# Kernel tuning notes

Measured on AMD Instinct MI355X. Metric: run time of the kernel, lower is better.

Reference implementation:

```python
import jax, jax.numpy as jnp
import numpy as np

B, S, H, F, E, K = 2, 2048, 1024, 4096, 8, 2


def setup_inputs() -> dict:
    key = jax.random.key(0)
    ks = jax.random.split(key, 6)
    x = jax.random.normal(ks[0], (B, S, H), dtype=jnp.float32)
    probs = jax.random.uniform(ks[1], (K, B, S, 1), dtype=jnp.float32)
    experts = jax.random.randint(ks[2], (K, B, S, 1), 0, E, dtype=jnp.int32)
    # per-expert FFN params; 0.02 scale mimics typical transformer init
    w1 = jax.random.normal(ks[3], (E, H, F), dtype=jnp.float32) * 0.02
    b1 = jnp.zeros((E, F), dtype=jnp.float32)
    w2 = jax.random.normal(ks[4], (E, F, H), dtype=jnp.float32) * 0.02
    b2 = jnp.zeros((E, H), dtype=jnp.float32)
    return {"x": x, "probs": probs, "experts": experts,
            "w1": w1, "b1": b1, "w2": w2, "b2": b2}


def reference(x, probs, experts, w1, b1, w2, b2):
    # Dense compute-all-experts FFN: every expert processes every token.
    h = jnp.einsum('bsh,ehf->ebsf', x, w1) + b1[:, None, None, :]  # [E,B,S,F]
    h = jax.nn.gelu(h)
    y = jnp.einsum('ebsf,efh->ebsh', h, w2) + b2[:, None, None, :]  # [E,B,S,H]
    # Masked combine: sum_e sum_j probs_j * y_e * (experts_j == e)
    onehot = jax.nn.one_hot(experts[..., 0], w1.shape[0], dtype=x.dtype)  # [K,B,S,E]
    weights = jnp.einsum('kbsl,kbse->bse', probs, onehot)  # [B,S,E]
    out = jnp.einsum('bse,ebsh->bsh', weights, y)
    return out
```

## Files before the change

### kernel.cpp

```cpp
#include <hip/hip_runtime.h>
#include <stdint.h>

#define H_DIM 1024
#define F_DIM 4096
#define E_NUM 8
#define T_NUM 4096
#define NE    8192
#define BM    256
#define BN    256
#define BK    64
#define MAXT  40
#define PADM  9984
#define TBY   65536
#define LDSSZ (2*TBY)

#define G1_NWG (MAXT * (F_DIM / BN))
#define TRW2_NWG 4096
#define TRW1_NWG 4096

#define M_NT  0
#define M_PB  1
#define M_CNT 16
#define M_CUR 24
#define M_TE  32
#define M_TR  72
#define M_INTS 112

typedef float  f32x4  __attribute__((ext_vector_type(4)));
typedef short  bf16x8 __attribute__((ext_vector_type(8)));
typedef __bf16 b16v8  __attribute__((ext_vector_type(8)));
typedef unsigned short u16;
typedef u16    u16x8  __attribute__((ext_vector_type(8)));

#define BAR()   __builtin_amdgcn_s_barrier()
#define FENCE() asm volatile("" ::: "memory")
#define LGKM0() asm volatile("s_waitcnt lgkmcnt(0)" ::: "memory")

__device__ __forceinline__ float gelu_tanh(float v) {
  float u = 0.7978845608028654f * (v + 0.044715f * v * v * v);
  return v / (1.0f + __expf(-2.0f * u));
}

__device__ __forceinline__ float b2f(u16 v) {
  union { float f; unsigned u; } x; x.u = ((unsigned)v) << 16; return x.f;
}

__device__ __forceinline__ void gl16(const void* g, void* l) {
  __builtin_amdgcn_global_load_lds(
      (const __attribute__((address_space(1))) unsigned int*)g,
      (__attribute__((address_space(3))) unsigned int*)l, 16, 0, 0);
}

__device__ __forceinline__ void trans_tile(const float* __restrict__ W, u16* __restrict__ Wt,
                                           int R, int C, int e, int bx, int by,
                                           char* L, int tid) {
  int r0 = by * 64, c0 = bx * 64;
  const float* We = W + (size_t)e * R * C;
  u16* Wte = Wt + (size_t)e * R * C;
#pragma unroll
  for (int it = 0; it < 4; ++it) {
    int gi = it * 256 + tid;
    int row = gi >> 4, c4 = gi & 15;
    f32x4 v = *(const f32x4*)(We + (size_t)(r0 + row) * C + c0 + c4 * 4);
    *(f32x4*)(L + row * 256 + ((c4 ^ (row & 15)) * 16)) = v;
  }
  __syncthreads();
#pragma unroll
  for (int s = 0; s < 2; ++s) {
    int chunk = s * 256 + tid;
    int c = chunk >> 3, rb = chunk & 7;
    b16v8 o;
#pragma unroll
    for (int j = 0; j < 8; ++j) {
      int r = rb * 8 + j;
      float f = *(const float*)(L + r * 256 + (((c >> 2) ^ (r & 15)) * 16) + (c & 3) * 4);
      o[j] = (__bf16)f;
    }
    *(b16v8*)(void*)(Wte + (size_t)(c0 + c) * R + r0 + rb * 8) = o;
  }
}


__global__ void k_init(int* tok, float* wgt, int* meta) {
  int i = blockIdx.x * 256 + threadIdx.x;
  if (i < PADM) { tok[i] = 0; wgt[i] = 0.f; }
  if (i < E_NUM) { meta[M_CNT + i] = 0; meta[M_CUR + i] = 0; }
}

__global__ void k_count(const int* __restrict__ experts, int* meta) {
  int i = blockIdx.x * 256 + threadIdx.x;
  int e = experts[i];
  int lane = threadIdx.x & 63;
#pragma unroll
  for (int ee = 0; ee < E_NUM; ++ee) {
    unsigned long long bm = __ballot(e == ee);
    if (e == ee && lane == __builtin_ctzll(bm))
      atomicAdd(&meta[M_CNT + ee], __popcll(bm));
  }
}

__global__ void k_plan(int* meta) {
  if (threadIdx.x != 0 || blockIdx.x != 0) return;
  int pb = 0, idx = 0;
  for (int e = 0; e < E_NUM; ++e) {
    int c = meta[M_CNT + e];
    int nt = (c + BM - 1) / BM;
    meta[M_PB + e] = pb;
    for (int t = 0; t < nt && idx < MAXT; ++t) {
      meta[M_TE + idx] = e; meta[M_TR + idx] = pb + t * BM; ++idx;
    }
    pb += nt * BM;
  }
  meta[M_NT] = idx;
}

__global__ void k_scatter(const int* __restrict__ experts, const float* __restrict__ probs,
                          int* tok, float* wgt, int* entpos, int* meta) {
  int i = blockIdx.x * 256 + threadIdx.x;
  int e = experts[i];
  int t = i & (T_NUM - 1);
  float p = probs[i];
  int lane = threadIdx.x & 63;
#pragma unroll
  for (int ee = 0; ee < E_NUM; ++ee) {
    unsigned long long bm = __ballot(e == ee);
    if (e == ee) {
      int leader = __builtin_ctzll(bm);
      int cnt = __popcll(bm);
      int base = 0;
      if (lane == leader) base = atomicAdd(&meta[M_CUR + ee], cnt);
      base = __shfl(base, leader);
      int rank = __popcll(bm & ((1ull << lane) - 1ull));
      int pos = meta[M_PB + ee] + base + rank;
      tok[pos] = t;
      wgt[pos] = p;
      entpos[i] = pos;
    }
  }
}

__global__ __launch_bounds__(512) void k_prep(const float* __restrict__ x, u16* __restrict__ xbf,
                                              const float* __restrict__ w1, u16* __restrict__ w1t) {
  int bid = blockIdx.x;
  if (bid < TRW1_NWG) {
    alignas(16) __shared__ char L[32768];
    int ti = bid * 2 + (threadIdx.x >> 8);
    int e = ti >> 10, rem = ti & 1023;
    int bx = rem & 63, by = rem >> 6;
    trans_tile(w1, w1t, H_DIM, F_DIM, e, bx, by, L + (threadIdx.x >> 8) * 16384, threadIdx.x & 255);
    return;
  }
  int i = (bid - TRW1_NWG) * 512 + threadIdx.x;
  const f32x4* xp = (const f32x4*)x;
  f32x4 a = xp[i * 2], b = xp[i * 2 + 1];
  b16v8 o;
  o[0] = (__bf16)a[0]; o[1] = (__bf16)a[1]; o[2] = (__bf16)a[2]; o[3] = (__bf16)a[3];
  o[4] = (__bf16)b[0]; o[5] = (__bf16)b[1]; o[6] = (__bf16)b[2]; o[7] = (__bf16)b[3];
  ((b16v8*)xbf)[i] = o;
}

__global__ __launch_bounds__(256) void k_trans(const float* __restrict__ W, u16* __restrict__ Wt,
                                               int R, int C) {
  alignas(16) __shared__ char L[16384];
  trans_tile(W, Wt, R, C, blockIdx.z, blockIdx.x, blockIdx.y, L, threadIdx.x);
}


#define STG_A(kt, dbb, h)                                                     \
  { gl16(asrc[2*(h)]   + (size_t)(kt) * BK, LDS + (dbb) + (2*(h))   * 8192 + wid * 1024); \
    gl16(asrc[2*(h)+1] + (size_t)(kt) * BK, LDS + (dbb) + (2*(h)+1) * 8192 + wid * 1024); }
#define STG_B(kt, dbb, h)                                                     \
  { gl16(bsrc[2*(h)]   + (size_t)(kt) * BK, LDS + (dbb) + 32768 + (2*(h))   * 8192 + wid * 1024); \
    gl16(bsrc[2*(h)+1] + (size_t)(kt) * BK, LDS + (dbb) + 32768 + (2*(h)+1) * 8192 + wid * 1024); }

#define LD_A(dst, mi, kk)                                                     \
  { int r_ = wr * 128 + (mi) * 16 + (lane & 15);                              \
    int kb_ = (kk) * 64 + ((lane >> 4) << 4);                                 \
    dst = *(const bf16x8*)(Ab_ + r_ * 128 + (kb_ ^ ((r_ & 7) << 4))); }
#define LD_B(dst, ni, kk)                                                     \
  { int c_ = wc * 64 + (ni) * 16 + (lane & 15);                               \
    int kb_ = (kk) * 64 + ((lane >> 4) << 4);                                 \
    dst = *(const bf16x8*)(Bb_ + c_ * 128 + (kb_ ^ ((c_ & 7) << 4))); }

#define MFMA16(p)                                                             \
  __builtin_amdgcn_s_setprio(1);                                              \
  _Pragma("unroll") for (int mm = 0; mm < 2; ++mm)                            \
    _Pragma("unroll") for (int n = 0; n < 4; ++n) {                           \
      acc[2*(p)+mm][n] = __builtin_amdgcn_mfma_f32_16x16x32_bf16(af[mm][0], bfr[n][0], acc[2*(p)+mm][n], 0, 0, 0); \
      acc[2*(p)+mm][n] = __builtin_amdgcn_mfma_f32_16x16x32_bf16(af[mm][1], bfr[n][1], acc[2*(p)+mm][n], 0, 0, 0); \
    }                                                                         \
  __builtin_amdgcn_s_setprio(0);

#define GEMM_KLOOP_8P(NT)                                                     \
  STG_A(0, 0, 0); STG_A(0, 0, 1); STG_B(0, 0, 0); STG_B(0, 0, 1);             \
  STG_B(1, TBY, 0); STG_B(1, TBY, 1);                                         \
  asm volatile("s_waitcnt vmcnt(4)" ::: "memory");                            \
  BAR();                                                                      \
  { int cur = 0;                                                              \
    for (int kt = 0; kt < (NT); ++kt) {                                       \
      const int db = cur * TBY, dn = (cur ^ 1) * TBY;                         \
      const char* Ab_ = LDS + db;                                             \
      const char* Bb_ = LDS + db + 32768;                                     \
      bf16x8 bfr[4][2], af[2][2];                                             \
                                                                 \
      FENCE();                                                                \
      _Pragma("unroll") for (int n = 0; n < 4; ++n) { LD_B(bfr[n][0], n, 0); LD_B(bfr[n][1], n, 1); } \
      LD_A(af[0][0], 0, 0); LD_A(af[0][1], 0, 1); LD_A(af[1][0], 1, 0); LD_A(af[1][1], 1, 1); \
      if (kt + 1 < (NT)) STG_A(kt + 1, dn, 0);                                \
      FENCE(); BAR(); LGKM0();                                                \
      MFMA16(0);                                                              \
      FENCE(); BAR();                                                         \
                                                                 \
      LD_A(af[0][0], 2, 0); LD_A(af[0][1], 2, 1); LD_A(af[1][0], 3, 0); LD_A(af[1][1], 3, 1); \
      if (kt + 1 < (NT)) STG_A(kt + 1, dn, 1);                                \
      FENCE(); BAR(); LGKM0();                                                \
      MFMA16(1);                                                              \
      FENCE(); BAR();                                                         \
                                                                 \
      LD_A(af[0][0], 4, 0); LD_A(af[0][1], 4, 1); LD_A(af[1][0], 5, 0); LD_A(af[1][1], 5, 1); \
      if (kt + 2 < (NT)) STG_B(kt + 2, db, 0);                                \
      FENCE(); BAR(); LGKM0();                                                \
      MFMA16(2);                                                              \
      FENCE(); BAR();                                                         \
                                                                 \
      LD_A(af[0][0], 6, 0); LD_A(af[0][1], 6, 1); LD_A(af[1][0], 7, 0); LD_A(af[1][1], 7, 1); \
      if (kt + 2 < (NT)) STG_B(kt + 2, db, 1);                                \
      FENCE(); BAR(); LGKM0();                                                \
      MFMA16(3);                                                              \
      FENCE();                                                                \
      if (kt == (NT) - 2)     { asm volatile("s_waitcnt vmcnt(0)" ::: "memory"); } \
      else if (kt < (NT) - 2) { asm volatile("s_waitcnt vmcnt(4)" ::: "memory"); } \
      BAR();                                                                  \
      cur ^= 1;                                                               \
    } }


__global__ __launch_bounds__(512, 1) void k_gemm1(
    const u16* __restrict__ xbf, const u16* __restrict__ w1t, const float* __restrict__ b1,
    const int* __restrict__ tok, const int* __restrict__ meta, u16* __restrict__ hbuf,
    const float* __restrict__ w2, u16* __restrict__ w2t)
{
  extern __shared__ char LDS[];
  int wg = blockIdx.x;
  if (wg >= G1_NWG) {
    int ti = (wg - G1_NWG) * 2 + (threadIdx.x >> 8);
    int e = ti >> 10, rem = ti & 1023;
    int bx = rem & 15, by = rem >> 4;
    trans_tile(w2, w2t, F_DIM, H_DIM, e, bx, by, LDS + (threadIdx.x >> 8) * 16384, threadIdx.x & 255);
    return;
  }
  int work = (wg & 7) * (G1_NWG / 8) + (wg >> 3);
  int slot = work % MAXT;
  int cbase = (work / MAXT) * BN;
  int nt = meta[M_NT];
  if (slot >= nt) return;
  int e     = meta[M_TE + slot];
  int rbase = meta[M_TR + slot];

  int tid = threadIdx.x;
  int lane = tid & 63;
  int wid = tid >> 6;
  int wr = wid >> 2, wc = wid & 3;
  int cc = tid & 7, rr = tid >> 3;

  const u16* asrc[4]; const u16* bsrc[4];
#pragma unroll
  for (int j = 0; j < 4; ++j) {
    int rj = j * 64 + rr;
    int t = tok[rbase + rj];
    asrc[j] = xbf + (size_t)t * H_DIM + ((cc ^ (rj & 7)) * 8);
    bsrc[j] = w1t + ((size_t)e * F_DIM + cbase + rj) * H_DIM + ((cc ^ (rj & 7)) * 8);
  }

  f32x4 acc[8][4];
#pragma unroll
  for (int m = 0; m < 8; ++m)
#pragma unroll
    for (int n = 0; n < 4; ++n) acc[m][n] = (f32x4){0.f, 0.f, 0.f, 0.f};

  GEMM_KLOOP_8P(H_DIM / BK)

  float bv[4];
#pragma unroll
  for (int n = 0; n < 4; ++n) bv[n] = b1[e * F_DIM + cbase + wc * 64 + n * 16 + (lane & 15)];
  char* reg = LDS + wid * 16384;
#pragma unroll
  for (int m = 0; m < 8; ++m)
#pragma unroll
    for (int n = 0; n < 4; ++n)
#pragma unroll
      for (int q = 0; q < 4; ++q) {
        float v = acc[m][n][q] + bv[n];
        v = gelu_tanh(v);
        int row4 = ((lane >> 4) << 2) + q;
        int col = n * 16 + (lane & 15);
        *(__bf16*)(reg + m * 2048 + row4 * 128 + col * 2) = (__bf16)v;
      }
#pragma unroll
  for (int q = 0; q < 16; ++q) {
    int m = q >> 1, p = q & 1;
    int byte = p * 1024 + lane * 16;
    u16x8 v = *(const u16x8*)(reg + m * 2048 + byte);
    int row  = p * 8 + (lane >> 3);
    int colb = (lane & 7) * 16;
    size_t grow = (size_t)(rbase + wr * 128 + m * 16 + row);
    size_t gcol = (size_t)(cbase + wc * 64 + (colb >> 1));
    *(u16x8*)(hbuf + grow * F_DIM + gcol) = v;
  }
}


template<int ZS>
__global__ __launch_bounds__(512, 1) void k_gemm2(
    const u16* __restrict__ hbuf, const u16* __restrict__ w2t, const float* __restrict__ b2,
    const int* __restrict__ meta, u16* __restrict__ ybuf)
{
  extern __shared__ char LDS[];
  const int NWG = MAXT * 4 * ZS;
  int wg = blockIdx.x;
  int work = (wg & 7) * (NWG / 8) + (wg >> 3);
  int zi   = work / (MAXT * 4);
  int rem  = work % (MAXT * 4);
  int slot = rem % MAXT;
  int cbase = (rem / MAXT) * BN;
  int kzb   = zi * (F_DIM / ZS);
  int nt = meta[M_NT];
  if (slot >= nt) return;
  int e     = meta[M_TE + slot];
  int rbase = meta[M_TR + slot];

  int tid = threadIdx.x;
  int lane = tid & 63;
  int wid = tid >> 6;
  int wr = wid >> 2, wc = wid & 3;
  int cc = tid & 7, rr = tid >> 3;

  const u16* asrc[4]; const u16* bsrc[4];
#pragma unroll
  for (int j = 0; j < 4; ++j) {
    int rj = j * 64 + rr;
    asrc[j] = hbuf + (size_t)(rbase + rj) * F_DIM + kzb + ((cc ^ (rj & 7)) * 8);
    bsrc[j] = w2t + ((size_t)e * H_DIM + cbase + rj) * F_DIM + kzb + ((cc ^ (rj & 7)) * 8);
  }

  f32x4 acc[8][4];
#pragma unroll
  for (int m = 0; m < 8; ++m)
#pragma unroll
    for (int n = 0; n < 4; ++n) acc[m][n] = (f32x4){0.f, 0.f, 0.f, 0.f};

  GEMM_KLOOP_8P((F_DIM / ZS) / BK)

  bool z0 = (zi == 0);
  u16* yb = ybuf + (size_t)zi * PADM * H_DIM;
  float bv[4];
#pragma unroll
  for (int n = 0; n < 4; ++n)
    bv[n] = z0 ? b2[e * H_DIM + cbase + wc * 64 + n * 16 + (lane & 15)] : 0.f;
  char* reg = LDS + wid * 16384;
#pragma unroll
  for (int m = 0; m < 8; ++m)
#pragma unroll
    for (int n = 0; n < 4; ++n)
#pragma unroll
      for (int q = 0; q < 4; ++q) {
        float v = acc[m][n][q] + bv[n];
        int row4 = ((lane >> 4) << 2) + q;
        int col = n * 16 + (lane & 15);
        *(__bf16*)(reg + m * 2048 + row4 * 128 + col * 2) = (__bf16)v;
      }
#pragma unroll
  for (int q = 0; q < 16; ++q) {
    int m = q >> 1, p = q & 1;
    int byte = p * 1024 + lane * 16;
    u16x8 v = *(const u16x8*)(reg + m * 2048 + byte);
    int row  = p * 8 + (lane >> 3);
    int colb = (lane & 7) * 16;
    size_t grow = (size_t)(rbase + wr * 128 + m * 16 + row);
    size_t gcol = (size_t)(cbase + wc * 64 + (colb >> 1));
    *(u16x8*)(yb + grow * H_DIM + gcol) = v;
  }
}


template<int ZS>
__global__ __launch_bounds__(256) void k_combine(
    const u16* __restrict__ ybuf, const float* __restrict__ wgt,
    const int* __restrict__ entpos, float* __restrict__ out)
{
  int idx = blockIdx.x * 256 + threadIdx.x;
  int t = idx >> 7, hc = idx & 127;
  int p0 = entpos[t], p1 = entpos[T_NUM + t];
  float w0 = wgt[p0], w1 = wgt[p1];
  float s0[8], s1[8];
#pragma unroll
  for (int j = 0; j < 8; ++j) { s0[j] = 0.f; s1[j] = 0.f; }
#pragma unroll
  for (int z = 0; z < ZS; ++z) {
    const u16x8* yz = (const u16x8*)(ybuf + (size_t)z * PADM * H_DIM);
    u16x8 a = yz[(size_t)p0 * (H_DIM / 8) + hc];
    u16x8 b = yz[(size_t)p1 * (H_DIM / 8) + hc];
#pragma unroll
    for (int j = 0; j < 8; ++j) { s0[j] += b2f(a[j]); s1[j] += b2f(b[j]); }
  }
  f32x4 o0, o1;
#pragma unroll
  for (int j = 0; j < 4; ++j) o0[j] = w0 * s0[j] + w1 * s1[j];
#pragma unroll
  for (int j = 0; j < 4; ++j) o1[j] = w0 * s0[4 + j] + w1 * s1[4 + j];
  f32x4* op = (f32x4*)(out + (size_t)t * H_DIM + hc * 8);
  op[0] = o0;
  op[1] = o1;
}


extern "C" void kernel_launch(void* const* d_in, const int* in_sizes, int n_in,
                              void* d_out, int out_size, void* d_ws, size_t ws_size,
                              hipStream_t stream)
{
  const float* x       = (const float*)d_in[0];
  const float* probs   = (const float*)d_in[1];
  const int*   experts = (const int*)d_in[2];
  const float* w1      = (const float*)d_in[3];
  const float* b1      = (const float*)d_in[4];
  const float* w2      = (const float*)d_in[5];
  const float* b2      = (const float*)d_in[6];
  float* out = (float*)d_out;

  char* ws = (char*)d_ws;
  size_t off = 0;
  u16*   hbuf = (u16*)(ws + off);  off += (size_t)PADM * F_DIM * sizeof(u16);
  u16*   xbf  = (u16*)(ws + off);  off += (size_t)T_NUM * H_DIM * sizeof(u16);
  u16*   w1t  = (u16*)(ws + off);  off += (size_t)E_NUM * F_DIM * H_DIM * sizeof(u16);
  u16*   ybuf = (u16*)(ws + off);  off += (size_t)2 * PADM * H_DIM * sizeof(u16);
  int*   tok  = (int*)(ws + off);  off += (size_t)PADM * sizeof(int);
  float* wgt  = (float*)(ws + off); off += (size_t)PADM * sizeof(float);
  int*   entpos = (int*)(ws + off); off += (size_t)NE * sizeof(int);
  int*   meta = (int*)(ws + off);  off += M_INTS * sizeof(int);
  size_t w2t_bytes = (size_t)E_NUM * F_DIM * H_DIM * sizeof(u16);
  bool fused = (ws_size >= off + w2t_bytes);
  u16* w2t = fused ? (u16*)(ws + off) : w1t;
  u16* ybuf4 = w1t;
  (void)in_sizes; (void)n_in;

  hipFuncSetAttribute(reinterpret_cast<const void*>(&k_gemm1),
                      hipFuncAttributeMaxDynamicSharedMemorySize, LDSSZ);
  hipFuncSetAttribute(reinterpret_cast<const void*>(&k_gemm2<4>),
                      hipFuncAttributeMaxDynamicSharedMemorySize, LDSSZ);
  hipFuncSetAttribute(reinterpret_cast<const void*>(&k_gemm2<2>),
                      hipFuncAttributeMaxDynamicSharedMemorySize, LDSSZ);

  k_init   <<<dim3((PADM + 255) / 256), 256, 0, stream>>>(tok, wgt, meta);
  k_count  <<<dim3(NE / 256), 256, 0, stream>>>(experts, meta);
  k_plan   <<<1, 1, 0, stream>>>(meta);
  k_scatter<<<dim3(NE / 256), 256, 0, stream>>>(experts, probs, tok, wgt, entpos, meta);
  k_prep   <<<dim3(TRW1_NWG + T_NUM * H_DIM / 8 / 512), 512, 0, stream>>>(x, xbf, w1, w1t);
  k_gemm1  <<<dim3(G1_NWG + (fused ? TRW2_NWG : 0)), 512, LDSSZ, stream>>>(
              xbf, w1t, b1, tok, meta, hbuf, w2, w2t);
  if (fused) {
    k_gemm2<4><<<dim3(MAXT * 4 * 4), 512, LDSSZ, stream>>>(hbuf, w2t, b2, meta, ybuf4);
    k_combine<4><<<dim3(T_NUM * H_DIM / 8 / 256), 256, 0, stream>>>(ybuf4, wgt, entpos, out);
  } else {
    k_trans<<<dim3(H_DIM / 64, F_DIM / 64, E_NUM), 256, 0, stream>>>(w2, w2t, F_DIM, H_DIM);
    k_gemm2<2><<<dim3(MAXT * 4 * 2), 512, LDSSZ, stream>>>(hbuf, w2t, b2, meta, ybuf);
    k_combine<2><<<dim3(T_NUM * H_DIM / 8 / 256), 256, 0, stream>>>(ybuf, wgt, entpos, out);
  }
}
```

Before: 321.7 us.

## Move W2 transpose into prep kernel and swizzle LDS epilogue staging

```diff
diff --git a/kernel.cpp b/kernel.cpp
--- a/kernel.cpp
+++ b/kernel.cpp
@@ -15,8 +15,9 @@
 #define LDSSZ (2*TBY)
 
 #define G1_NWG (MAXT * (F_DIM / BN))
+#define TRW1_NWG 4096
 #define TRW2_NWG 4096
-#define TRW1_NWG 4096
+#define CVT_NWG  (T_NUM * H_DIM / 8 / 512)
 
 #define M_NT  0
 #define M_PB  1
@@ -140,7 +141,9 @@
 }
 
 __global__ __launch_bounds__(512) void k_prep(const float* __restrict__ x, u16* __restrict__ xbf,
-                                              const float* __restrict__ w1, u16* __restrict__ w1t) {
+                                              const float* __restrict__ w1, u16* __restrict__ w1t,
+                                              const float* __restrict__ w2, u16* __restrict__ w2t,
+                                              int nw2blk) {
   int bid = blockIdx.x;
   if (bid < TRW1_NWG) {
     alignas(16) __shared__ char L[32768];
@@ -150,7 +153,15 @@
     trans_tile(w1, w1t, H_DIM, F_DIM, e, bx, by, L + (threadIdx.x >> 8) * 16384, threadIdx.x & 255);
     return;
   }
-  int i = (bid - TRW1_NWG) * 512 + threadIdx.x;
+  if (bid < TRW1_NWG + nw2blk) {
+    alignas(16) __shared__ char L[32768];
+    int ti = (bid - TRW1_NWG) * 2 + (threadIdx.x >> 8);
+    int e = ti >> 10, rem = ti & 1023;
+    int bx = rem & 15, by = rem >> 4;
+    trans_tile(w2, w2t, F_DIM, H_DIM, e, bx, by, L + (threadIdx.x >> 8) * 16384, threadIdx.x & 255);
+    return;
+  }
+  int i = (bid - TRW1_NWG - nw2blk) * 512 + threadIdx.x;
   const f32x4* xp = (const f32x4*)x;
   f32x4 a = xp[i * 2], b = xp[i * 2 + 1];
   b16v8 o;
@@ -237,18 +248,10 @@
 
 __global__ __launch_bounds__(512, 1) void k_gemm1(
     const u16* __restrict__ xbf, const u16* __restrict__ w1t, const float* __restrict__ b1,
-    const int* __restrict__ tok, const int* __restrict__ meta, u16* __restrict__ hbuf,
-    const float* __restrict__ w2, u16* __restrict__ w2t)
+    const int* __restrict__ tok, const int* __restrict__ meta, u16* __restrict__ hbuf)
 {
   extern __shared__ char LDS[];
   int wg = blockIdx.x;
-  if (wg >= G1_NWG) {
-    int ti = (wg - G1_NWG) * 2 + (threadIdx.x >> 8);
-    int e = ti >> 10, rem = ti & 1023;
-    int bx = rem & 15, by = rem >> 4;
-    trans_tile(w2, w2t, F_DIM, H_DIM, e, bx, by, LDS + (threadIdx.x >> 8) * 16384, threadIdx.x & 255);
-    return;
-  }
   int work = (wg & 7) * (G1_NWG / 8) + (wg >> 3);
   int slot = work % MAXT;
   int cbase = (work / MAXT) * BN;
@@ -294,15 +297,14 @@
         v = gelu_tanh(v);
         int row4 = ((lane >> 4) << 2) + q;
         int col = n * 16 + (lane & 15);
-        *(__bf16*)(reg + m * 2048 + row4 * 128 + col * 2) = (__bf16)v;
+        *(__bf16*)(reg + m * 2048 + row4 * 128 + ((col * 2) ^ ((row4 >> 2) << 5))) = (__bf16)v;
       }
 #pragma unroll
   for (int q = 0; q < 16; ++q) {
     int m = q >> 1, p = q & 1;
-    int byte = p * 1024 + lane * 16;
-    u16x8 v = *(const u16x8*)(reg + m * 2048 + byte);
     int row  = p * 8 + (lane >> 3);
     int colb = (lane & 7) * 16;
+    u16x8 v = *(const u16x8*)(reg + m * 2048 + row * 128 + (colb ^ ((row >> 2) << 5)));
     size_t grow = (size_t)(rbase + wr * 128 + m * 16 + row);
     size_t gcol = (size_t)(cbase + wc * 64 + (colb >> 1));
     *(u16x8*)(hbuf + grow * F_DIM + gcol) = v;
@@ -367,15 +369,14 @@
         float v = acc[m][n][q] + bv[n];
         int row4 = ((lane >> 4) << 2) + q;
         int col = n * 16 + (lane & 15);
-        *(__bf16*)(reg + m * 2048 + row4 * 128 + col * 2) = (__bf16)v;
+        *(__bf16*)(reg + m * 2048 + row4 * 128 + ((col * 2) ^ ((row4 >> 2) << 5))) = (__bf16)v;
       }
 #pragma unroll
   for (int q = 0; q < 16; ++q) {
     int m = q >> 1, p = q & 1;
-    int byte = p * 1024 + lane * 16;
-    u16x8 v = *(const u16x8*)(reg + m * 2048 + byte);
     int row  = p * 8 + (lane >> 3);
     int colb = (lane & 7) * 16;
+    u16x8 v = *(const u16x8*)(reg + m * 2048 + row * 128 + (colb ^ ((row >> 2) << 5)));
     size_t grow = (size_t)(rbase + wr * 128 + m * 16 + row);
     size_t gcol = (size_t)(cbase + wc * 64 + (colb >> 1));
     *(u16x8*)(yb + grow * H_DIM + gcol) = v;
@@ -450,13 +451,15 @@
   hipFuncSetAttribute(reinterpret_cast<const void*>(&k_gemm2<2>),
                       hipFuncAttributeMaxDynamicSharedMemorySize, LDSSZ);
 
+  int nw2blk = fused ? TRW2_NWG : 0;
+
   k_init   <<<dim3((PADM + 255) / 256), 256, 0, stream>>>(tok, wgt, meta);
   k_count  <<<dim3(NE / 256), 256, 0, stream>>>(experts, meta);
   k_plan   <<<1, 1, 0, stream>>>(meta);
   k_scatter<<<dim3(NE / 256), 256, 0, stream>>>(experts, probs, tok, wgt, entpos, meta);
-  k_prep   <<<dim3(TRW1_NWG + T_NUM * H_DIM / 8 / 512), 512, 0, stream>>>(x, xbf, w1, w1t);
-  k_gemm1  <<<dim3(G1_NWG + (fused ? TRW2_NWG : 0)), 512, LDSSZ, stream>>>(
-              xbf, w1t, b1, tok, meta, hbuf, w2, w2t);
+  k_prep   <<<dim3(TRW1_NWG + nw2blk + CVT_NWG), 512, 0, stream>>>(
+              x, xbf, w1, w1t, w2, w2t, nw2blk);
+  k_gemm1  <<<dim3(G1_NWG), 512, LDSSZ, stream>>>(xbf, w1t, b1, tok, meta, hbuf);
   if (fused) {
     k_gemm2<4><<<dim3(MAXT * 4 * 4), 512, LDSSZ, stream>>>(hbuf, w2t, b2, meta, ybuf4);
     k_combine<4><<<dim3(T_NUM * H_DIM / 8 / 256), 256, 0, stream>>>(ybuf4, wgt, entpos, out);
```

New measurement: 339.2 us. +5.5%, slower.
